# Kernel optimization log

Measured on AMD Instinct MI355X. Metric: run time of the kernel, lower is better.

## Reference

```python
import jax, jax.numpy as jnp
import numpy as np

EMBED_DIM = 1024
NUM_HEADS = 16
HEAD_DIM = EMBED_DIM // NUM_HEADS
BATCH = 2
SEQ = 2048


def setup_inputs() -> dict:
    key = jax.random.key(0)
    ks = jax.random.split(key, 9)
    s = 1.0 / np.sqrt(EMBED_DIM)
    return {
        "x": jax.random.normal(ks[0], (BATCH, SEQ, EMBED_DIM), jnp.float32),
        "mask": jnp.ones((BATCH, SEQ), jnp.int32),
        "Wq": jax.random.normal(ks[1], (EMBED_DIM, EMBED_DIM), jnp.float32) * s,
        "bq": jax.random.normal(ks[2], (EMBED_DIM,), jnp.float32) * s,
        "Wk": jax.random.normal(ks[3], (EMBED_DIM, EMBED_DIM), jnp.float32) * s,
        "bk": jax.random.normal(ks[4], (EMBED_DIM,), jnp.float32) * s,
        "Wv": jax.random.normal(ks[5], (EMBED_DIM, EMBED_DIM), jnp.float32) * s,
        "bv": jax.random.normal(ks[6], (EMBED_DIM,), jnp.float32) * s,
        "Wo": jax.random.normal(ks[7], (EMBED_DIM, EMBED_DIM), jnp.float32) * s,
        "bo": jax.random.normal(ks[8], (EMBED_DIM,), jnp.float32) * s,
    }


def reference(x, mask, Wq, bq, Wk, bk, Wv, bv, Wo, bo):
    B, S, E = x.shape
    H, D = NUM_HEADS, HEAD_DIM
    # torch Linear: y = x @ W.T + b
    q = (x @ Wq.T + bq).reshape(B, S, H, D).transpose(0, 2, 1, 3)  # [B,H,S,D]
    k = (x @ Wk.T + bk).reshape(B, S, H, D).transpose(0, 2, 1, 3)
    v = (x @ Wv.T + bv).reshape(B, S, H, D).transpose(0, 2, 1, 3)
    scores = jnp.einsum("bhqd,bhkd->bhqk", q, k) / jnp.sqrt(jnp.float32(D))
    # mask: [B,S] -> [B,1,1,S]; fill masked positions with -1e9
    scores = jnp.where(mask[:, None, None, :] == 0, jnp.float32(-1e9), scores)
    probs = jax.nn.softmax(scores, axis=-1)
    # dropout omitted: original stores a float and would crash; eval semantics = identity
    attn = jnp.einsum("bhqk,bhkd->bhqd", probs, v)  # [B,H,S,D]
    attn = attn.transpose(0, 2, 1, 3).reshape(B, S, E)
    return attn @ Wo.T + bo
```

## Files before the change

### kernel.cpp

```cpp
#include <hip/hip_runtime.h>
#include <stdint.h>

#define S_LEN 2048
#define EMB   1024
#define NH    16
#define HD    64
#define BK 64

typedef __bf16 bf16x8 __attribute__((ext_vector_type(8)));
typedef short  short4v __attribute__((ext_vector_type(4)));
typedef unsigned int uint2v __attribute__((ext_vector_type(2)));
typedef float  floatx4 __attribute__((ext_vector_type(4)));

#if defined(__has_builtin)
#if __has_builtin(__builtin_amdgcn_mfma_f32_16x16x16bf16_1k)
#define HAVE_MFMA16 1
#endif
#if __has_builtin(__builtin_amdgcn_exp2f)
#define EXP2F __builtin_amdgcn_exp2f
#endif
#endif
#ifndef EXP2F
#define EXP2F exp2f
#endif

#define QSCALE 0.1803368801111204f

__device__ __forceinline__ unsigned short f2bf(float f) {
  unsigned u = __builtin_bit_cast(unsigned, f);
  u += 0x7fffu + ((u >> 16) & 1u);
  return (unsigned short)(u >> 16);
}
__device__ __forceinline__ unsigned short f2bf_hu(float f) {
  return (unsigned short)((__builtin_bit_cast(unsigned, f) + 0x8000u) >> 16);
}
__device__ __forceinline__ unsigned packbf2(float a, float b) {
  unsigned ua = __builtin_bit_cast(unsigned, a) + 0x8000u;
  unsigned ub = __builtin_bit_cast(unsigned, b) + 0x8000u;
  return __builtin_amdgcn_perm(ub, ua, 0x07060302);
}

__global__ __launch_bounds__(256) void cvt_all(const float* __restrict__ x,
                                               const float* __restrict__ Wq,
                                               const float* __restrict__ Wk,
                                               const float* __restrict__ Wv,
                                               const float* __restrict__ Wo,
                                               unsigned short* __restrict__ xb,
                                               unsigned short* __restrict__ Wqb,
                                               unsigned short* __restrict__ Wkb,
                                               unsigned short* __restrict__ Wvb,
                                               unsigned short* __restrict__ Wob) {
  int blk = blockIdx.x;
  const float* s; unsigned short* d; int off;
  if (blk < 4096)      { s = x;  d = xb;  off = blk; }
  else if (blk < 5120) { s = Wq; d = Wqb; off = blk - 4096; }
  else if (blk < 6144) { s = Wk; d = Wkb; off = blk - 5120; }
  else if (blk < 7168) { s = Wv; d = Wvb; off = blk - 6144; }
  else                 { s = Wo; d = Wob; off = blk - 7168; }
  int i = (off * 256 + threadIdx.x) * 4;
  float4 v = *(const float4*)(s + i);
  ushort4 o;
  o.x = f2bf(v.x); o.y = f2bf(v.y); o.z = f2bf(v.z); o.w = f2bf(v.w);
  *(ushort4*)(d + i) = o;
}

__device__ __forceinline__ void stage16(const void* g, void* l) {
  __builtin_amdgcn_global_load_lds(
      (const __attribute__((address_space(1))) void*)g,
      (__attribute__((address_space(3))) void*)l, 16, 0, 0);
}

__global__ __launch_bounds__(256, 4) void qkv_gemm(const unsigned short* __restrict__ xb,
                                                   const unsigned short* __restrict__ Wqb,
                                                   const unsigned short* __restrict__ Wkb,
                                                   const unsigned short* __restrict__ Wvb,
                                                   const float* __restrict__ bq,
                                                   const float* __restrict__ bk,
                                                   const float* __restrict__ bv,
                                                   unsigned short* __restrict__ Qb,
                                                   unsigned short* __restrict__ Kb,
                                                   unsigned short* __restrict__ Vtb) {
  __shared__ unsigned short As[64 * BK];
  __shared__ unsigned short Bs[128 * BK];
  const int z = blockIdx.z;
  const unsigned short* Bm = (z == 0) ? Wqb : (z == 1) ? Wkb : Wvb;
  const float* bias        = (z == 0) ? bq  : (z == 1) ? bk  : bv;
  unsigned short* outp     = (z == 0) ? Qb  : (z == 1) ? Kb  : Vtb;
  const float scale = (z == 0) ? QSCALE : 1.0f;
  const int mode = (z == 2) ? 2 : 1;

  const int tid  = threadIdx.x;
  const int lane = tid & 63;
  const int wave = tid >> 6;
  const int m16  = lane & 15;
  const int quad = lane >> 4;
  const int m0 = blockIdx.x * 64;
  const int n0 = blockIdx.y * 128;
  const int wrow = (wave >> 1) * 32;
  const int wcol = (wave & 1) * 64;
  const int K = 1024;

  floatx4 acc[2][4];
  for (int i = 0; i < 2; ++i)
    for (int j = 0; j < 4; ++j) acc[i][j] = floatx4{0.f, 0.f, 0.f, 0.f};

  for (int k0 = 0; k0 < K; k0 += BK) {
    __syncthreads();
    for (int i = 0; i < 2; ++i) {
      int c = i * 256 + tid;
      int row = c >> 3, col = (c & 7) << 3;
      stage16(xb + (size_t)(m0 + row) * K + k0 + col,
              (char*)As + (size_t)(i * 256 + wave * 64) * 16);
    }
    for (int i = 0; i < 4; ++i) {
      int c = i * 256 + tid;
      int row = c >> 3, col = (c & 7) << 3;
      stage16(Bm + (size_t)(n0 + row) * K + k0 + col,
              (char*)Bs + (size_t)(i * 256 + wave * 64) * 16);
    }
    __syncthreads();
    for (int kk = 0; kk < 2; ++kk) {
      bf16x8 af[2], bfr[4];
      for (int ti = 0; ti < 2; ++ti)
        af[ti] = *(const bf16x8*)(As + (wrow + ti * 16 + m16) * BK + kk * 32 + quad * 8);
      for (int tj = 0; tj < 4; ++tj)
        bfr[tj] = *(const bf16x8*)(Bs + (wcol + tj * 16 + m16) * BK + kk * 32 + quad * 8);
      for (int ti = 0; ti < 2; ++ti)
        for (int tj = 0; tj < 4; ++tj)
          acc[ti][tj] = __builtin_amdgcn_mfma_f32_16x16x32_bf16(bfr[tj], af[ti], acc[ti][tj], 0, 0, 0);
    }
  }

  if (mode == 1) {
    for (int ti = 0; ti < 2; ++ti) {
      int m = m0 + wrow + ti * 16 + m16;
      int b = m >> 11, ss = m & 2047;
      for (int tj = 0; tj < 4; ++tj) {
        int n = n0 + wcol + tj * 16 + quad * 4;
        int hh = n >> 6, d = n & 63;
        float4 b4 = *(const float4*)(bias + n);
        float v0 = (acc[ti][tj][0] + b4.x) * scale;
        float v1 = (acc[ti][tj][1] + b4.y) * scale;
        float v2 = (acc[ti][tj][2] + b4.z) * scale;
        float v3 = (acc[ti][tj][3] + b4.w) * scale;
        uint2v pk{packbf2(v0, v1), packbf2(v2, v3)};
        *(uint2v*)((unsigned short*)outp +
                   ((size_t)(b * NH + hh) * S_LEN + ss) * HD + d) = pk;
      }
    }
  } else {
    for (int tj = 0; tj < 4; ++tj)
      for (int reg = 0; reg < 4; ++reg) {
        int n = n0 + wcol + tj * 16 + quad * 4 + reg;
        int hh = n >> 6, d = n & 63;
        float bv = bias[n];
        for (int ti = 0; ti < 2; ++ti) {
          int m = m0 + wrow + ti * 16 + m16;
          int b = m >> 11, ss = m & 2047;
          ((unsigned short*)outp)[((size_t)(b * NH + hh) * HD + d) * S_LEN + ss] =
              f2bf_hu(acc[ti][tj][reg] + bv);
        }
      }
  }
}

__global__ __launch_bounds__(256, 4) void out_gemm(const unsigned short* __restrict__ Ab,
                                                   const unsigned short* __restrict__ Wob,
                                                   const float* __restrict__ bo,
                                                   float* __restrict__ out) {
  __shared__ unsigned short As[64 * BK];
  __shared__ unsigned short Bs[64 * BK];
  const int tid  = threadIdx.x;
  const int lane = tid & 63;
  const int wave = tid >> 6;
  const int m16  = lane & 15;
  const int quad = lane >> 4;
  const int m0 = blockIdx.x * 64;
  const int n0 = blockIdx.y * 64;
  const int wrow = (wave >> 1) * 32;
  const int wcol = (wave & 1) * 32;
  const int K = 1024, N = 1024;

  floatx4 acc[2][2];
  for (int i = 0; i < 2; ++i)
    for (int j = 0; j < 2; ++j) acc[i][j] = floatx4{0.f, 0.f, 0.f, 0.f};

  for (int k0 = 0; k0 < K; k0 += BK) {
    __syncthreads();
    for (int i = 0; i < 2; ++i) {
      int c = i * 256 + tid;
      int row = c >> 3, col = (c & 7) << 3;
      stage16(Ab + (size_t)(m0 + row) * K + k0 + col,
              (char*)As + (size_t)(i * 256 + wave * 64) * 16);
      stage16(Wob + (size_t)(n0 + row) * K + k0 + col,
              (char*)Bs + (size_t)(i * 256 + wave * 64) * 16);
    }
    __syncthreads();
    for (int kk = 0; kk < 2; ++kk) {
      bf16x8 af[2], bfr[2];
      for (int ti = 0; ti < 2; ++ti)
        af[ti] = *(const bf16x8*)(As + (wrow + ti * 16 + m16) * BK + kk * 32 + quad * 8);
      for (int tj = 0; tj < 2; ++tj)
        bfr[tj] = *(const bf16x8*)(Bs + (wcol + tj * 16 + m16) * BK + kk * 32 + quad * 8);
      for (int ti = 0; ti < 2; ++ti)
        for (int tj = 0; tj < 2; ++tj)
          acc[ti][tj] = __builtin_amdgcn_mfma_f32_16x16x32_bf16(af[ti], bfr[tj], acc[ti][tj], 0, 0, 0);
    }
  }

  for (int tj = 0; tj < 2; ++tj) {
    int n = n0 + wcol + tj * 16 + m16;
    float bv = bo[n];
    for (int ti = 0; ti < 2; ++ti)
      for (int reg = 0; reg < 4; ++reg) {
        int m = m0 + wrow + ti * 16 + quad * 4 + reg;
        out[(size_t)m * N + n] = acc[ti][tj][reg] + bv;
      }
  }
}

__global__ __launch_bounds__(512, 2) void attn_kernel(const unsigned short* __restrict__ Qb,
                                                      const unsigned short* __restrict__ Kb,
                                                      const unsigned short* __restrict__ Vtb,
                                                      const int* __restrict__ mask,
                                                      unsigned short* __restrict__ attnb) {
  __shared__ unsigned short Ks[2 * 128 * 64];
  __shared__ unsigned short Vts[2 * 64 * 128];
  __shared__ int zw[8];
#ifndef HAVE_MFMA16
  __shared__ unsigned short Pq[8 * 16 * 72];
#endif

  const int tid  = threadIdx.x;
  const int lane = tid & 63;
  const int wave = tid >> 6;
  const int m16  = lane & 15;
  const int quad = lane >> 4;
  const int bh = blockIdx.x;
  const int qt = blockIdx.y;
  const int b  = bh >> 4;
  const int h  = bh & 15;
  const int q0 = qt * 128;
  const size_t head = (size_t)bh * S_LEN * HD;

  bf16x8 qf[2];
  {
    const unsigned short* qrow = Qb + head + (size_t)(q0 + wave * 16 + m16) * HD;
    qf[0] = *(const bf16x8*)(qrow + quad * 8);
    qf[1] = *(const bf16x8*)(qrow + 32 + quad * 8);
  }

  const int krow = tid >> 3, kch = tid & 7;
  const unsigned short* kg = Kb + head + (size_t)krow * HD + kch * 8;
  const int kloff = krow * 64 + ((kch ^ (krow & 7)) << 3);
  const int vrow = tid >> 4, vch = tid & 15;
  const unsigned short* vg = Vtb + head + (size_t)vrow * S_LEN + vch * 8;
  const int vloff = vrow * 128 + ((vch ^ (vrow & 7)) << 3);
  const int* mrow = mask + b * S_LEN;

  float l_run = 0.f;
  floatx4 acc_o[4];
  for (int ti = 0; ti < 4; ++ti) acc_o[ti] = floatx4{0.f, 0.f, 0.f, 0.f};

  {
    int4 mv = *(const int4*)(mrow + tid * 4);
    bool z = (mv.x & mv.y & mv.z & mv.w) == 0;
    unsigned long long bal = __ballot(z);
    if (lane == 0) zw[wave] = (bal != 0ull) ? 1 : 0;
  }

  uint4 kp0 = *(const uint4*)(kg);
  uint4 kp1 = *(const uint4*)(kg + 64 * HD);
  uint4 vp0 = *(const uint4*)(vg);
  uint4 vp1 = *(const uint4*)(vg + 32 * S_LEN);
  *(uint4*)&Ks[kloff] = kp0;  *(uint4*)&Ks[64 * 64 + kloff] = kp1;
  *(uint4*)&Vts[vloff] = vp0; *(uint4*)&Vts[32 * 128 + vloff] = vp1;
  kp0 = *(const uint4*)(kg + 128 * HD);
  kp1 = *(const uint4*)(kg + 192 * HD);
  vp0 = *(const uint4*)(vg + 128);
  vp1 = *(const uint4*)(vg + 32 * S_LEN + 128);
  __syncthreads();
  const bool anymask = (zw[0] | zw[1] | zw[2] | zw[3] | zw[4] | zw[5] | zw[6] | zw[7]) != 0;

  const int xs = m16 & 7;
  const floatx4 fz = floatx4{0.f, 0.f, 0.f, 0.f};

  for (int kb = 0; kb < 16; ++kb) {
    const int p = kb & 1;
    const unsigned short* Kp = Ks + p * (128 * 64);
    const unsigned short* Vp = Vts + p * (64 * 128);
    if (kb < 15) {
      unsigned short* Kn = Ks + (p ^ 1) * (128 * 64);
      unsigned short* Vn = Vts + (p ^ 1) * (64 * 128);
      *(uint4*)&Kn[kloff] = kp0;  *(uint4*)&Kn[64 * 64 + kloff] = kp1;
      *(uint4*)&Vn[vloff] = vp0;  *(uint4*)&Vn[32 * 128 + vloff] = vp1;
      int kvn = (kb + 2 < 16) ? (kb + 2) * 128 : 0;
      kp0 = *(const uint4*)(kg + (size_t)kvn * HD);
      kp1 = *(const uint4*)(kg + (size_t)(kvn + 64) * HD);
      vp0 = *(const uint4*)(vg + kvn);
      vp1 = *(const uint4*)(vg + 32 * S_LEN + kvn);
    }

    for (int hf = 0; hf < 2; ++hf) {
      floatx4 acc_s[4];
      for (int tj = 0; tj < 4; ++tj) {
        bf16x8 kf0 = *(const bf16x8*)&Kp[(hf * 64 + tj * 16 + m16) * 64 + ((quad ^ xs) << 3)];
        acc_s[tj] = __builtin_amdgcn_mfma_f32_16x16x32_bf16(kf0, qf[0], fz, 0, 0, 0);
      }
      for (int tj = 0; tj < 4; ++tj) {
        bf16x8 kf1 = *(const bf16x8*)&Kp[(hf * 64 + tj * 16 + m16) * 64 + (((4 + quad) ^ xs) << 3)];
        acc_s[tj] = __builtin_amdgcn_mfma_f32_16x16x32_bf16(kf1, qf[1], acc_s[tj], 0, 0, 0);
      }

      float sv[16];
      for (int t = 0; t < 4; ++t)
        for (int r = 0; r < 4; ++r) sv[t * 4 + r] = acc_s[t][r];
      if (anymask) {
        for (int t = 0; t < 4; ++t)
          for (int r = 0; r < 4; ++r) {
            int idx = kb * 128 + hf * 64 + t * 16 + quad * 4 + r;
            sv[t * 4 + r] += (mrow[idx] == 0) ? -1e9f : 0.f;
          }
      }

      unsigned up[8];
      float sl = 0.f;
      for (int i = 0; i < 8; ++i) {
        float p0 = EXP2F(sv[2 * i]);
        float p1 = EXP2F(sv[2 * i + 1]);
        sl += p0 + p1;
        up[i] = packbf2(p0, p1);
      }
      sl += __shfl_xor(sl, 16);
      sl += __shfl_xor(sl, 32);
      l_run += sl;

#ifdef HAVE_MFMA16
      for (int ti = 0; ti < 4; ++ti)
        for (int c = 0; c < 4; ++c) {
          short4v vf = *(const short4v*)&Vp[(ti * 16 + m16) * 128 +
                                            (((hf * 8 + 2 * c + (quad >> 1)) ^ xs) << 3) +
                                            ((quad & 1) << 2)];
          short4v Pb = __builtin_bit_cast(short4v, uint2v{up[2 * c], up[2 * c + 1]});
          acc_o[ti] = __builtin_amdgcn_mfma_f32_16x16x16bf16_1k(vf, Pb, acc_o[ti], 0, 0, 0);
        }
#else
      unsigned short* Pw = Pq + wave * 16 * 72;
      for (int t = 0; t < 4; ++t) {
        *(unsigned*)&Pw[m16 * 72 + t * 16 + quad * 4]     = up[2 * t];
        *(unsigned*)&Pw[m16 * 72 + t * 16 + quad * 4 + 2] = up[2 * t + 1];
      }
      for (int kk = 0; kk < 2; ++kk) {
        bf16x8 pf = *(const bf16x8*)&Pw[m16 * 72 + kk * 32 + quad * 8];
        for (int ti = 0; ti < 4; ++ti) {
          bf16x8 vf = *(const bf16x8*)&Vp[(ti * 16 + m16) * 128 +
                                          (((hf * 8 + kk * 4 + quad) ^ xs) << 3)];
          acc_o[ti] = __builtin_amdgcn_mfma_f32_16x16x32_bf16(vf, pf, acc_o[ti], 0, 0, 0);
        }
      }
#endif
    }

    __syncthreads();
  }

  float rl = 1.f / l_run;
  int orow = q0 + wave * 16 + m16;
  for (int ti = 0; ti < 4; ++ti) {
    ushort4 o;
    o.x = f2bf_hu(acc_o[ti][0] * rl);
    o.y = f2bf_hu(acc_o[ti][1] * rl);
    o.z = f2bf_hu(acc_o[ti][2] * rl);
    o.w = f2bf_hu(acc_o[ti][3] * rl);
    int e = h * HD + ti * 16 + quad * 4;
    *(ushort4*)&attnb[((size_t)(b * S_LEN + orow)) * EMB + e] = o;
  }
}

extern "C" void kernel_launch(void* const* d_in, const int* in_sizes, int n_in,
                              void* d_out, int out_size, void* d_ws, size_t ws_size,
                              hipStream_t stream) {
  const float* x  = (const float*)d_in[0];
  const int* mask = (const int*)d_in[1];
  const float* Wq = (const float*)d_in[2];
  const float* bq = (const float*)d_in[3];
  const float* Wk = (const float*)d_in[4];
  const float* bk = (const float*)d_in[5];
  const float* Wv = (const float*)d_in[6];
  const float* bv = (const float*)d_in[7];
  const float* Wo = (const float*)d_in[8];
  const float* bo = (const float*)d_in[9];
  float* out = (float*)d_out;

  char* ws = (char*)d_ws;
  unsigned short* xb  = (unsigned short*)(ws);
  unsigned short* Wqb = (unsigned short*)(ws + 8388608);
  unsigned short* Wkb = (unsigned short*)(ws + 10485760);
  unsigned short* Wvb = (unsigned short*)(ws + 12582912);
  unsigned short* Wob = (unsigned short*)(ws + 14680064);
  unsigned short* Qb  = (unsigned short*)(ws + 16777216);
  unsigned short* Kbb = (unsigned short*)(ws + 25165824);
  unsigned short* Vtb = (unsigned short*)(ws + 33554432);
  unsigned short* Ab  = (unsigned short*)(ws + 41943040);

  cvt_all<<<dim3(8192), dim3(256), 0, stream>>>(x, Wq, Wk, Wv, Wo, xb, Wqb, Wkb, Wvb, Wob);
  qkv_gemm<<<dim3(64, 8, 3), dim3(256), 0, stream>>>(xb, Wqb, Wkb, Wvb, bq, bk, bv, Qb, Kbb, Vtb);
  attn_kernel<<<dim3(32, 16), dim3(512), 0, stream>>>(Qb, Kbb, Vtb, mask, Ab);
  out_gemm<<<dim3(64, 16), dim3(256), 0, stream>>>(Ab, Wob, bo, out);
}
```

Measured before the change: 210.0 us.

## Give each attention wave two query tiles and stage K/V via direct-to-LDS loads

```diff
diff --git a/kernel.cpp b/kernel.cpp
--- a/kernel.cpp
+++ b/kernel.cpp
@@ -219,16 +219,16 @@
   }
 }
 
-__global__ __launch_bounds__(512, 2) void attn_kernel(const unsigned short* __restrict__ Qb,
+__global__ __launch_bounds__(256, 2) void attn_kernel(const unsigned short* __restrict__ Qb,
                                                       const unsigned short* __restrict__ Kb,
                                                       const unsigned short* __restrict__ Vtb,
                                                       const int* __restrict__ mask,
                                                       unsigned short* __restrict__ attnb) {
   __shared__ unsigned short Ks[2 * 128 * 64];
   __shared__ unsigned short Vts[2 * 64 * 128];
-  __shared__ int zw[8];
+  __shared__ int zw[4];
 #ifndef HAVE_MFMA16
-  __shared__ unsigned short Pq[8 * 16 * 72];
+  __shared__ unsigned short Pq[4 * 16 * 72];
 #endif
 
   const int tid  = threadIdx.x;
@@ -243,44 +243,54 @@
   const int q0 = qt * 128;
   const size_t head = (size_t)bh * S_LEN * HD;
 
-  bf16x8 qf[2];
+  bf16x8 qf[2][2];
+  for (int qs = 0; qs < 2; ++qs) {
+    const unsigned short* qrow = Qb + head + (size_t)(q0 + wave * 32 + qs * 16 + m16) * HD;
+    qf[qs][0] = *(const bf16x8*)(qrow + quad * 8);
+    qf[qs][1] = *(const bf16x8*)(qrow + 32 + quad * 8);
+  }
+
+  const int kr = lane >> 3, kc = lane & 7;
+  const unsigned short* kg0 = Kb + head + (size_t)(wave * 32 + kr) * HD + ((kc ^ (kr & 7)) << 3);
+  const int vd = lane >> 4;
+  const int vce = (lane & 8) | ((lane & 7) ^ vd);
+  const unsigned short* vg0 = Vtb + head + (size_t)(wave * 16 + vd) * S_LEN + (vce << 3);
+  const unsigned short* vg1 = Vtb + head + (size_t)(wave * 16 + 4 + vd) * S_LEN + ((vce ^ 4) << 3);
+  const int* mrow = mask + b * S_LEN;
+
+#define STAGE_KV(pp, kb_)                                                      \
+  {                                                                            \
+    const unsigned short* ksrc = kg0 + (size_t)(kb_) * 128 * HD;               \
+    char* kdst = (char*)Ks + (pp) * 16384 + wave * 4096;                       \
+    stage16(ksrc,        kdst);                                                \
+    stage16(ksrc + 512,  kdst + 1024);                                         \
+    stage16(ksrc + 1024, kdst + 2048);                                         \
+    stage16(ksrc + 1536, kdst + 3072);                                         \
+    const unsigned short* ve = vg0 + (kb_) * 128;                              \
+    const unsigned short* vo = vg1 + (kb_) * 128;                              \
+    char* vdst = (char*)Vts + (pp) * 16384 + wave * 4096;                      \
+    stage16(ve,             vdst);                                             \
+    stage16(vo,             vdst + 1024);                                      \
+    stage16(ve + 8 * S_LEN, vdst + 2048);                                      \
+    stage16(vo + 8 * S_LEN, vdst + 3072);                                      \
+  }
+
+  float l_run[2] = {0.f, 0.f};
+  floatx4 acc_o[2][4];
+  for (int qs = 0; qs < 2; ++qs)
+    for (int ti = 0; ti < 4; ++ti) acc_o[qs][ti] = floatx4{0.f, 0.f, 0.f, 0.f};
+
   {
-    const unsigned short* qrow = Qb + head + (size_t)(q0 + wave * 16 + m16) * HD;
-    qf[0] = *(const bf16x8*)(qrow + quad * 8);
-    qf[1] = *(const bf16x8*)(qrow + 32 + quad * 8);
-  }
-
-  const int krow = tid >> 3, kch = tid & 7;
-  const unsigned short* kg = Kb + head + (size_t)krow * HD + kch * 8;
-  const int kloff = krow * 64 + ((kch ^ (krow & 7)) << 3);
-  const int vrow = tid >> 4, vch = tid & 15;
-  const unsigned short* vg = Vtb + head + (size_t)vrow * S_LEN + vch * 8;
-  const int vloff = vrow * 128 + ((vch ^ (vrow & 7)) << 3);
-  const int* mrow = mask + b * S_LEN;
-
-  float l_run = 0.f;
-  floatx4 acc_o[4];
-  for (int ti = 0; ti < 4; ++ti) acc_o[ti] = floatx4{0.f, 0.f, 0.f, 0.f};
-
-  {
-    int4 mv = *(const int4*)(mrow + tid * 4);
-    bool z = (mv.x & mv.y & mv.z & mv.w) == 0;
+    const int4* mp = (const int4*)(mrow + tid * 8);
+    int4 a = mp[0], c4 = mp[1];
+    bool z = (a.x & a.y & a.z & a.w & c4.x & c4.y & c4.z & c4.w) == 0;
     unsigned long long bal = __ballot(z);
     if (lane == 0) zw[wave] = (bal != 0ull) ? 1 : 0;
   }
 
-  uint4 kp0 = *(const uint4*)(kg);
-  uint4 kp1 = *(const uint4*)(kg + 64 * HD);
-  uint4 vp0 = *(const uint4*)(vg);
-  uint4 vp1 = *(const uint4*)(vg + 32 * S_LEN);
-  *(uint4*)&Ks[kloff] = kp0;  *(uint4*)&Ks[64 * 64 + kloff] = kp1;
-  *(uint4*)&Vts[vloff] = vp0; *(uint4*)&Vts[32 * 128 + vloff] = vp1;
-  kp0 = *(const uint4*)(kg + 128 * HD);
-  kp1 = *(const uint4*)(kg + 192 * HD);
-  vp0 = *(const uint4*)(vg + 128);
-  vp1 = *(const uint4*)(vg + 32 * S_LEN + 128);
+  STAGE_KV(0, 0);
   __syncthreads();
-  const bool anymask = (zw[0] | zw[1] | zw[2] | zw[3] | zw[4] | zw[5] | zw[6] | zw[7]) != 0;
+  const bool anymask = (zw[0] | zw[1] | zw[2] | zw[3]) != 0;
 
   const int xs = m16 & 7;
   const floatx4 fz = floatx4{0.f, 0.f, 0.f, 0.f};
@@ -289,51 +299,49 @@
     const int p = kb & 1;
     const unsigned short* Kp = Ks + p * (128 * 64);
     const unsigned short* Vp = Vts + p * (64 * 128);
-    if (kb < 15) {
-      unsigned short* Kn = Ks + (p ^ 1) * (128 * 64);
-      unsigned short* Vn = Vts + (p ^ 1) * (64 * 128);
-      *(uint4*)&Kn[kloff] = kp0;  *(uint4*)&Kn[64 * 64 + kloff] = kp1;
-      *(uint4*)&Vn[vloff] = vp0;  *(uint4*)&Vn[32 * 128 + vloff] = vp1;
-      int kvn = (kb + 2 < 16) ? (kb + 2) * 128 : 0;
-      kp0 = *(const uint4*)(kg + (size_t)kvn * HD);
-      kp1 = *(const uint4*)(kg + (size_t)(kvn + 64) * HD);
-      vp0 = *(const uint4*)(vg + kvn);
-      vp1 = *(const uint4*)(vg + 32 * S_LEN + kvn);
-    }
+    if (kb < 15) STAGE_KV(p ^ 1, kb + 1);
 
     for (int hf = 0; hf < 2; ++hf) {
-      floatx4 acc_s[4];
-      for (int tj = 0; tj < 4; ++tj) {
-        bf16x8 kf0 = *(const bf16x8*)&Kp[(hf * 64 + tj * 16 + m16) * 64 + ((quad ^ xs) << 3)];
-        acc_s[tj] = __builtin_amdgcn_mfma_f32_16x16x32_bf16(kf0, qf[0], fz, 0, 0, 0);
-      }
-      for (int tj = 0; tj < 4; ++tj) {
-        bf16x8 kf1 = *(const bf16x8*)&Kp[(hf * 64 + tj * 16 + m16) * 64 + (((4 + quad) ^ xs) << 3)];
-        acc_s[tj] = __builtin_amdgcn_mfma_f32_16x16x32_bf16(kf1, qf[1], acc_s[tj], 0, 0, 0);
-      }
-
-      float sv[16];
-      for (int t = 0; t < 4; ++t)
-        for (int r = 0; r < 4; ++r) sv[t * 4 + r] = acc_s[t][r];
-      if (anymask) {
+      floatx4 acc_s[2][4];
+      {
+        bf16x8 kf[4];
+        for (int tj = 0; tj < 4; ++tj)
+          kf[tj] = *(const bf16x8*)&Kp[(hf * 64 + tj * 16 + m16) * 64 + ((quad ^ xs) << 3)];
+        for (int tj = 0; tj < 4; ++tj) {
+          acc_s[0][tj] = __builtin_amdgcn_mfma_f32_16x16x32_bf16(kf[tj], qf[0][0], fz, 0, 0, 0);
+          acc_s[1][tj] = __builtin_amdgcn_mfma_f32_16x16x32_bf16(kf[tj], qf[1][0], fz, 0, 0, 0);
+        }
+        for (int tj = 0; tj < 4; ++tj)
+          kf[tj] = *(const bf16x8*)&Kp[(hf * 64 + tj * 16 + m16) * 64 + (((4 + quad) ^ xs) << 3)];
+        for (int tj = 0; tj < 4; ++tj) {
+          acc_s[0][tj] = __builtin_amdgcn_mfma_f32_16x16x32_bf16(kf[tj], qf[0][1], acc_s[0][tj], 0, 0, 0);
+          acc_s[1][tj] = __builtin_amdgcn_mfma_f32_16x16x32_bf16(kf[tj], qf[1][1], acc_s[1][tj], 0, 0, 0);
+        }
+      }
+
+      unsigned up[2][8];
+      for (int qs = 0; qs < 2; ++qs) {
+        float sv[16];
         for (int t = 0; t < 4; ++t)
-          for (int r = 0; r < 4; ++r) {
-            int idx = kb * 128 + hf * 64 + t * 16 + quad * 4 + r;
-            sv[t * 4 + r] += (mrow[idx] == 0) ? -1e9f : 0.f;
-          }
-      }
-
-      unsigned up[8];
-      float sl = 0.f;
-      for (int i = 0; i < 8; ++i) {
-        float p0 = EXP2F(sv[2 * i]);
-        float p1 = EXP2F(sv[2 * i + 1]);
-        sl += p0 + p1;
-        up[i] = packbf2(p0, p1);
-      }
-      sl += __shfl_xor(sl, 16);
-      sl += __shfl_xor(sl, 32);
-      l_run += sl;
+          for (int r = 0; r < 4; ++r) sv[t * 4 + r] = acc_s[qs][t][r];
+        if (anymask) {
+          for (int t = 0; t < 4; ++t)
+            for (int r = 0; r < 4; ++r) {
+              int idx = kb * 128 + hf * 64 + t * 16 + quad * 4 + r;
+              sv[t * 4 + r] += (mrow[idx] == 0) ? -1e9f : 0.f;
+            }
+        }
+        float sl = 0.f;
+        for (int i = 0; i < 8; ++i) {
+          float p0 = EXP2F(sv[2 * i]);
+          float p1 = EXP2F(sv[2 * i + 1]);
+          sl += p0 + p1;
+          up[qs][i] = packbf2(p0, p1);
+        }
+        sl += __shfl_xor(sl, 16);
+        sl += __shfl_xor(sl, 32);
+        l_run[qs] += sl;
+      }
 
 #ifdef HAVE_MFMA16
       for (int ti = 0; ti < 4; ++ti)
@@ -341,21 +349,27 @@
           short4v vf = *(const short4v*)&Vp[(ti * 16 + m16) * 128 +
                                             (((hf * 8 + 2 * c + (quad >> 1)) ^ xs) << 3) +
                                             ((quad & 1) << 2)];
-          short4v Pb = __builtin_bit_cast(short4v, uint2v{up[2 * c], up[2 * c + 1]});
-          acc_o[ti] = __builtin_amdgcn_mfma_f32_16x16x16bf16_1k(vf, Pb, acc_o[ti], 0, 0, 0);
+          short4v Pb0 = __builtin_bit_cast(short4v, uint2v{up[0][2 * c], up[0][2 * c + 1]});
+          short4v Pb1 = __builtin_bit_cast(short4v, uint2v{up[1][2 * c], up[1][2 * c + 1]});
+          acc_o[0][ti] = __builtin_amdgcn_mfma_f32_16x16x16bf16_1k(vf, Pb0, acc_o[0][ti], 0, 0, 0);
+          acc_o[1][ti] = __builtin_amdgcn_mfma_f32_16x16x16bf16_1k(vf, Pb1, acc_o[1][ti], 0, 0, 0);
         }
 #else
-      unsigned short* Pw = Pq + wave * 16 * 72;
-      for (int t = 0; t < 4; ++t) {
-        *(unsigned*)&Pw[m16 * 72 + t * 16 + quad * 4]     = up[2 * t];
-        *(unsigned*)&Pw[m16 * 72 + t * 16 + quad * 4 + 2] = up[2 * t + 1];
-      }
-      for (int kk = 0; kk < 2; ++kk) {
-        bf16x8 pf = *(const bf16x8*)&Pw[m16 * 72 + kk * 32 + quad * 8];
-        for (int ti = 0; ti < 4; ++ti) {
-          bf16x8 vf = *(const bf16x8*)&Vp[(ti * 16 + m16) * 128 +
-                                          (((hf * 8 + kk * 4 + quad) ^ xs) << 3)];
-          acc_o[ti] = __builtin_amdgcn_mfma_f32_16x16x32_bf16(vf, pf, acc_o[ti], 0, 0, 0);
+      {
+        unsigned short* Pw = Pq + wave * 16 * 72;
+        for (int qs = 0; qs < 2; ++qs) {
+          for (int t = 0; t < 4; ++t) {
+            *(unsigned*)&Pw[m16 * 72 + t * 16 + quad * 4]     = up[qs][2 * t];
+            *(unsigned*)&Pw[m16 * 72 + t * 16 + quad * 4 + 2] = up[qs][2 * t + 1];
+          }
+          for (int kk = 0; kk < 2; ++kk) {
+            bf16x8 pf = *(const bf16x8*)&Pw[m16 * 72 + kk * 32 + quad * 8];
+            for (int ti = 0; ti < 4; ++ti) {
+              bf16x8 vfb = *(const bf16x8*)&Vp[(ti * 16 + m16) * 128 +
+                                               (((hf * 8 + kk * 4 + quad) ^ xs) << 3)];
+              acc_o[qs][ti] = __builtin_amdgcn_mfma_f32_16x16x32_bf16(vfb, pf, acc_o[qs][ti], 0, 0, 0);
+            }
+          }
         }
       }
 #endif
@@ -364,17 +378,20 @@
     __syncthreads();
   }
 
-  float rl = 1.f / l_run;
-  int orow = q0 + wave * 16 + m16;
-  for (int ti = 0; ti < 4; ++ti) {
-    ushort4 o;
-    o.x = f2bf_hu(acc_o[ti][0] * rl);
-    o.y = f2bf_hu(acc_o[ti][1] * rl);
-    o.z = f2bf_hu(acc_o[ti][2] * rl);
-    o.w = f2bf_hu(acc_o[ti][3] * rl);
-    int e = h * HD + ti * 16 + quad * 4;
-    *(ushort4*)&attnb[((size_t)(b * S_LEN + orow)) * EMB + e] = o;
-  }
+  for (int qs = 0; qs < 2; ++qs) {
+    float rl = 1.f / l_run[qs];
+    int orow = q0 + wave * 32 + qs * 16 + m16;
+    for (int ti = 0; ti < 4; ++ti) {
+      ushort4 o;
+      o.x = f2bf_hu(acc_o[qs][ti][0] * rl);
+      o.y = f2bf_hu(acc_o[qs][ti][1] * rl);
+      o.z = f2bf_hu(acc_o[qs][ti][2] * rl);
+      o.w = f2bf_hu(acc_o[qs][ti][3] * rl);
+      int e = h * HD + ti * 16 + quad * 4;
+      *(ushort4*)&attnb[((size_t)(b * S_LEN + orow)) * EMB + e] = o;
+    }
+  }
+#undef STAGE_KV
 }
 
 extern "C" void kernel_launch(void* const* d_in, const int* in_sizes, int n_in,
@@ -405,6 +422,6 @@
 
   cvt_all<<<dim3(8192), dim3(256), 0, stream>>>(x, Wq, Wk, Wv, Wo, xb, Wqb, Wkb, Wvb, Wob);
   qkv_gemm<<<dim3(64, 8, 3), dim3(256), 0, stream>>>(xb, Wqb, Wkb, Wvb, bq, bk, bv, Qb, Kbb, Vtb);
-  attn_kernel<<<dim3(32, 16), dim3(512), 0, stream>>>(Qb, Kbb, Vtb, mask, Ab);
+  attn_kernel<<<dim3(32, 16), dim3(256), 0, stream>>>(Qb, Kbb, Vtb, mask, Ab);
   out_gemm<<<dim3(64, 16), dim3(256), 0, stream>>>(Ab, Wob, bo, out);
 }
```

Result: no change. 206.1 us (-1.9%).
